# Performance work log

Measured on AMD Instinct MI355X. Metric: run time of the kernel, lower is better.

The kernel has to match this reference:

```python
import jax, jax.numpy as jnp
import numpy as np

B, S, D, H = 4, 1024, 1024, 16
HD = D // H
MAX_DIST, WIN, MAX_SPAN = 512, 256, 512
TEMP_SCALE = 0.01
EPS = 1e-5


def _ln(x, g, b):
    m = x.mean(-1, keepdims=True)
    v = ((x - m) ** 2).mean(-1, keepdims=True)
    return (x - m) * jax.lax.rsqrt(v + EPS) * g + b


def _heads(t):
    b, s, _ = t.shape
    return t.reshape(b, s, H, HD).transpose(0, 2, 1, 3)


def _merge(t):
    b, _, s, _ = t.shape
    return t.transpose(0, 2, 1, 3).reshape(b, s, D)


def _global_attn(x, Wq, bq, Wk, Wv, bv, Wo, bo):
    # MultiheadC with mask tensor passed -> is_causal=True SDPA (default 1/sqrt(HD) scale)
    q = _heads(x @ Wq.T + bq)
    k = _heads(x @ Wk.T)
    v = _heads(x @ Wv.T + bv)
    s = jnp.einsum('bhqd,bhkd->bhqk', q, k) / float(np.sqrt(HD))
    n = x.shape[1]
    causal = jnp.tril(jnp.ones((n, n), bool))
    s = jnp.where(causal, s, jnp.finfo(s.dtype).min)
    w = jax.nn.softmax(s, axis=-1)
    return _merge(jnp.einsum('bhqk,bhkd->bhqd', w, v)) @ Wo.T + bo


def _span_attn(q, k, v, temp):
    # AdaptiveSpan core: softmax(QK^T / temperature * head_dim**-0.25) V
    scale = HD ** -0.25
    qh, kh, vh = _heads(q), _heads(k), _heads(v)
    w = jax.nn.softmax(jnp.einsum('bhqd,bhkd->bhqk', qh, kh) / temp * scale, axis=-1)
    return _merge(jnp.einsum('bhqk,bhkd->bhqd', w, vh))


def _slide_win(local, span_mean, win, span_len, local_max):
    bx, sx, dx = local.shape
    temp = 1.0 + TEMP_SCALE * (1.0 - span_mean)  # sharpen=True branch
    outs = []
    for st in range(0, sx, win):  # static unrolled loop over windows (ragged slices)
        en = min(st + win, sx)
        wlen = en - st
        ks = max(0, st - span_len + win)
        ke = min(st + span_len, sx)
        klen = ke - ks
        eff = min(int(wlen * span_mean), wlen, klen, local_max)
        if eff <= 0:
            outs.append(jnp.zeros((bx, wlen, dx), local.dtype))
            continue
        o = _span_attn(local[:, st:st + eff], local[:, ks:ks + eff], local[:, ks:ks + eff], temp)
        if eff < wlen:
            o = jnp.concatenate([o, jnp.zeros((bx, wlen - eff, dx), local.dtype)], axis=1)
        outs.append(o)
    return jnp.concatenate(outs, axis=1)


def setup_inputs() -> dict:
    key = jax.random.key(0)
    ks = jax.random.split(key, 8)
    qkv_std = 1.0 / float(np.sqrt(HD))
    return {
        'x': jax.random.normal(ks[0], (B, S, D), jnp.float32),
        'ln_a_g': jnp.ones((D,), jnp.float32),
        'ln_a_b': jnp.zeros((D,), jnp.float32),
        'ln_b_g': jnp.ones((D,), jnp.float32),
        'ln_b_b': jnp.zeros((D,), jnp.float32),
        'Wq': jax.random.normal(ks[1], (D, D), jnp.float32) * qkv_std,
        'bq': jnp.zeros((D,), jnp.float32),
        'Wk': jax.random.normal(ks[2], (D, D), jnp.float32) * qkv_std,
        'Wv': jax.random.normal(ks[3], (D, D), jnp.float32) * qkv_std,
        'bv': jnp.zeros((D,), jnp.float32),
        'Wo': jax.random.normal(ks[4], (D, D), jnp.float32) * 0.02,
        'bo': jnp.zeros((D,), jnp.float32),
        'Wp': jax.random.normal(ks[5], (1, D), jnp.float32) * float(np.sqrt(2.0 / (D + 1))),
        'bp': jnp.zeros((1,), jnp.float32),
        'Wproj': jax.random.normal(ks[6], (D, 2 * D), jnp.float32) * 0.02,
        'bproj': jnp.zeros((D,), jnp.float32),
    }


def reference(x, ln_a_g, ln_a_b, ln_b_g, ln_b_b, Wq, bq, Wk, Wv, bv, Wo, bo, Wp, bp, Wproj, bproj):
    local = _ln(x, ln_a_g, ln_a_b)
    globe = _ln(x, ln_b_g, ln_b_b)
    globe_out = _global_attn(globe, Wq, bq, Wk, Wv, bv, Wo, bo)
    # Predictor: sigmoid(Linear(mean over seq))
    base_scale = jax.nn.sigmoid(globe_out.mean(axis=1) @ Wp.T + bp)  # [B, 1]
    span_scale = jnp.clip(base_scale, 0.0, 1.0)  # RL refine factor fixed at 1.0 (deterministic)
    span_mean = float(jnp.mean(span_scale))  # mirrors torch .item() host sync
    win = max(1, int(WIN * span_mean))
    span_len = max(1, int(MAX_SPAN * span_mean))
    local_max = min(MAX_DIST, span_len, win)
    local_out = _slide_win(local, span_mean, win, span_len, local_max)
    combined = jnp.concatenate([local_out, globe_out], axis=-1)
    return combined @ Wproj.T + bproj
```

## Files before the change

kernel.cpp:

```cpp
#include <hip/hip_runtime.h>
#include <math.h>

#define B_ 4
#define S_ 1024
#define D_ 1024
#define H_ 16
#define HD_ 64
#define BSD_ (B_*S_*D_)

using short8 = __attribute__((ext_vector_type(8))) short;
using f32x4  = __attribute__((ext_vector_type(4))) float;

#define MFMA16(a,b,c) __builtin_amdgcn_mfma_f32_16x16x32_bf16((a),(b),(c),0,0,0)

__device__ __forceinline__ ushort f2bf(float f) {
  uint u = __float_as_uint(f);
  return (ushort)((u + 0x7fffu + ((u >> 16) & 1u)) >> 16);
}
__device__ __forceinline__ float bf2f(ushort h) {
  return __uint_as_float(((uint)h) << 16);
}
__device__ __forceinline__ void split8(const float* p, short8* hi, short8* lo) {
  #pragma unroll
  for (int j = 0; j < 8; j++) {
    ushort h = f2bf(p[j]);
    (*hi)[j] = (short)h;
    (*lo)[j] = (short)f2bf(p[j] - bf2f(h));
  }
}
__device__ __forceinline__ void async_load16(const ushort* g, ushort* l) {
  __builtin_amdgcn_global_load_lds(
      (const __attribute__((address_space(1))) unsigned int*)g,
      (__attribute__((address_space(3))) unsigned int*)l, 16, 0, 0);
}

__device__ __forceinline__ float block_reduce_sum_256(float v, float* sbuf) {
  #pragma unroll
  for (int off = 32; off > 0; off >>= 1) v += __shfl_xor(v, off, 64);
  int lane = threadIdx.x & 63, wid = threadIdx.x >> 6;
  __syncthreads();
  if (lane == 0) sbuf[wid] = v;
  __syncthreads();
  return sbuf[0] + sbuf[1] + sbuf[2] + sbuf[3];
}

__global__ __launch_bounds__(256) void ln_kernel(const float* __restrict__ x,
                                                 const float* __restrict__ g,
                                                 const float* __restrict__ bta,
                                                 float* __restrict__ out) {
  __shared__ float sbuf[4];
  const int row = blockIdx.x;
  const float* xr = x + (size_t)row * D_;
  const int t = threadIdx.x;
  float v[4]; float s = 0.f;
  #pragma unroll
  for (int i = 0; i < 4; i++) { v[i] = xr[t + 256*i]; s += v[i]; }
  const float mean = block_reduce_sum_256(s, sbuf) * (1.0f/D_);
  float sq = 0.f;
  #pragma unroll
  for (int i = 0; i < 4; i++) { float d = v[i]-mean; sq += d*d; }
  const float var = block_reduce_sum_256(sq, sbuf) * (1.0f/D_);
  const float r = rsqrtf(var + 1e-5f);
  float* orow = out + (size_t)row * D_;
  #pragma unroll
  for (int i = 0; i < 4; i++) {
    int c = t + 256*i;
    orow[c] = (v[i]-mean)*r*g[c] + bta[c];
  }
}

__global__ __launch_bounds__(256) void ln_split_kernel(const float* __restrict__ x,
                                                       const float* __restrict__ g,
                                                       const float* __restrict__ bta,
                                                       ushort* __restrict__ out) {
  __shared__ float sbuf[4];
  const int row = blockIdx.x;
  const int t = threadIdx.x;
  const int c = t*4;
  const float* xr = x + (size_t)row * D_;
  float4 v = *(const float4*)(xr + c);
  float s = v.x + v.y + v.z + v.w;
  const float mean = block_reduce_sum_256(s, sbuf) * (1.0f/D_);
  float4 dv = make_float4(v.x-mean, v.y-mean, v.z-mean, v.w-mean);
  float sq = dv.x*dv.x + dv.y*dv.y + dv.z*dv.z + dv.w*dv.w;
  const float var = block_reduce_sum_256(sq, sbuf) * (1.0f/D_);
  const float r = rsqrtf(var + 1e-5f);
  float4 gg = *(const float4*)(g + c);
  float4 bb = *(const float4*)(bta + c);
  float n[4];
  n[0] = dv.x*r*gg.x + bb.x; n[1] = dv.y*r*gg.y + bb.y;
  n[2] = dv.z*r*gg.z + bb.z; n[3] = dv.w*r*gg.w + bb.w;
  ushort4 hi, lo;
  hi.x = f2bf(n[0]); hi.y = f2bf(n[1]); hi.z = f2bf(n[2]); hi.w = f2bf(n[3]);
  lo.x = f2bf(n[0]-bf2f(hi.x)); lo.y = f2bf(n[1]-bf2f(hi.y));
  lo.z = f2bf(n[2]-bf2f(hi.z)); lo.w = f2bf(n[3]-bf2f(hi.w));
  ushort* orow = out + (size_t)row*2048;
  *(ushort4*)(orow + c)        = hi;
  *(ushort4*)(orow + 1024 + c) = lo;
}

__global__ __launch_bounds__(256) void split_act_kernel(const float* __restrict__ in,
                                                        ushort* __restrict__ out) {
  const int idx = blockIdx.x*256 + threadIdx.x;
  const int row = idx >> 8;
  const int col4 = (idx & 255) << 2;
  const float4 a = *(const float4*)(in + (size_t)row*1024 + col4);
  ushort4 hi, lo;
  hi.x = f2bf(a.x); hi.y = f2bf(a.y); hi.z = f2bf(a.z); hi.w = f2bf(a.w);
  lo.x = f2bf(a.x - bf2f(hi.x)); lo.y = f2bf(a.y - bf2f(hi.y));
  lo.z = f2bf(a.z - bf2f(hi.z)); lo.w = f2bf(a.w - bf2f(hi.w));
  ushort* orow = out + (size_t)row*2048;
  *(ushort4*)(orow + col4)        = hi;
  *(ushort4*)(orow + 1024 + col4) = lo;
}

__global__ __launch_bounds__(256) void split_w3_kernel(const float* __restrict__ Wq,
                                                       const float* __restrict__ Wk,
                                                       const float* __restrict__ Wv,
                                                       const float* __restrict__ bq,
                                                       const float* __restrict__ bv,
                                                       ushort* __restrict__ out,
                                                       float* __restrict__ biascat) {
  const int idx = blockIdx.x*256 + threadIdx.x;
  const int n = idx >> 8;
  const int col4 = (idx & 255) << 2;
  const float* src = (n < 1024) ? (Wq + (size_t)n*1024)
                   : (n < 2048) ? (Wk + (size_t)(n-1024)*1024)
                                : (Wv + (size_t)(n-2048)*1024);
  const float4 a = *(const float4*)(src + col4);
  ushort4 hi, lo;
  hi.x = f2bf(a.x); hi.y = f2bf(a.y); hi.z = f2bf(a.z); hi.w = f2bf(a.w);
  lo.x = f2bf(a.x - bf2f(hi.x)); lo.y = f2bf(a.y - bf2f(hi.y));
  lo.z = f2bf(a.z - bf2f(hi.z)); lo.w = f2bf(a.w - bf2f(hi.w));
  ushort* orow = out + (size_t)n*2048;
  *(ushort4*)(orow + col4)        = hi;
  *(ushort4*)(orow + 1024 + col4) = lo;
  if (idx < 3072)
    biascat[idx] = (idx < 1024) ? bq[idx] : (idx < 2048) ? 0.f : bv[idx-2048];
}

__global__ __launch_bounds__(256) void split_w1_kernel(const float* __restrict__ W,
                                                       ushort* __restrict__ out) {
  const int idx = blockIdx.x*256 + threadIdx.x;
  const int n = idx >> 8;
  const int col4 = (idx & 255) << 2;
  const float4 a = *(const float4*)(W + (size_t)n*1024 + col4);
  ushort4 hi, lo;
  hi.x = f2bf(a.x); hi.y = f2bf(a.y); hi.z = f2bf(a.z); hi.w = f2bf(a.w);
  lo.x = f2bf(a.x - bf2f(hi.x)); lo.y = f2bf(a.y - bf2f(hi.y));
  lo.z = f2bf(a.z - bf2f(hi.z)); lo.w = f2bf(a.w - bf2f(hi.w));
  ushort* orow = out + (size_t)n*2048;
  *(ushort4*)(orow + col4)        = hi;
  *(ushort4*)(orow + 1024 + col4) = lo;
}

__global__ __launch_bounds__(256) void cvt_bf16_kernel(const float* __restrict__ in,
                                                       ushort* __restrict__ out,
                                                       int gprshift, int ostride, int ooff) {
  const int idx = blockIdx.x*256 + threadIdx.x;
  const int row = idx >> gprshift;
  const int col4 = (idx & ((1 << gprshift) - 1)) << 2;
  const int ncols = 4 << gprshift;
  const float4 a = *(const float4*)(in + (size_t)row*ncols + col4);
  ushort4 hi;
  hi.x = f2bf(a.x); hi.y = f2bf(a.y); hi.z = f2bf(a.z); hi.w = f2bf(a.w);
  *(ushort4*)(out + (size_t)row*ostride + ooff + col4) = hi;
}

__global__ __launch_bounds__(256) void mfma_gemm_qkv(
    const ushort* __restrict__ A, const ushort* __restrict__ Bw,
    const float* __restrict__ bias,
    ushort* __restrict__ Qsp, ushort* __restrict__ Ksp,
    ushort* __restrict__ Vth, ushort* __restrict__ Vtl, int Kh) {
  __shared__ __align__(16) ushort smem[17408];
  ushort* Ash = smem;
  ushort* Asl = smem + 4096;
  ushort* Bsh = smem + 8192;
  ushort* Bsl = smem + 12288;
  const int lda = 2*Kh;
  const int tid = threadIdx.x;
  const int bm = blockIdx.y * 128, bn = blockIdx.x * 128;
  const int wave = tid >> 6, lane = tid & 63;
  const int wm = wave >> 1, wn = wave & 1;
  const int lm = lane & 15, q = lane >> 4;
  const int lrow = lane >> 2;
  const int sw = (((lane & 3) ^ ((lane >> 3) & 3)) << 3);

  f32x4 acc[4][4];
  #pragma unroll
  for (int i = 0; i < 4; i++)
    #pragma unroll
    for (int j = 0; j < 4; j++)
      acc[i][j] = (f32x4){0.f,0.f,0.f,0.f};

  const ushort* Agh = A  + (size_t)(bm + wave*32 + lrow)*lda + sw;
  const ushort* Agl = Agh + Kh;
  const ushort* Bgh = Bw + (size_t)(bn + wave*32 + lrow)*lda + sw;
  const ushort* Bgl = Bgh + Kh;
  const size_t r16a = (size_t)16*lda;
  ushort* AhD0 = &Ash[(wave*32)*32];      ushort* AhD1 = &Ash[(wave*32+16)*32];
  ushort* AlD0 = &Asl[(wave*32)*32];      ushort* AlD1 = &Asl[(wave*32+16)*32];
  ushort* BhD0 = &Bsh[(wave*32)*32];      ushort* BhD1 = &Bsh[(wave*32+16)*32];
  ushort* BlD0 = &Bsl[(wave*32)*32];      ushort* BlD1 = &Bsl[(wave*32+16)*32];
  const int rsw  = ((q ^ ((lm >> 1) & 3)) << 3);
  const int aoff = (wm*64 + lm)*32 + rsw;
  const int boff = (wn*64 + lm)*32 + rsw;

  for (int k0 = 0; k0 < Kh; k0 += 32) {
    __syncthreads();
    async_load16(Agh + k0, AhD0);
    async_load16(Agh + r16a + k0, AhD1);
    async_load16(Agl + k0, AlD0);
    async_load16(Agl + r16a + k0, AlD1);
    async_load16(Bgh + k0, BhD0);
    async_load16(Bgh + r16a + k0, BhD1);
    async_load16(Bgl + k0, BlD0);
    async_load16(Bgl + r16a + k0, BlD1);
    __syncthreads();
    short8 ah[4], al[4], bh[4], bl[4];
    #pragma unroll
    for (int mt = 0; mt < 4; mt++) {
      ah[mt] = *(const short8*)&Ash[aoff + mt*512];
      al[mt] = *(const short8*)&Asl[aoff + mt*512];
    }
    #pragma unroll
    for (int nt = 0; nt < 4; nt++) {
      bh[nt] = *(const short8*)&Bsh[boff + nt*512];
      bl[nt] = *(const short8*)&Bsl[boff + nt*512];
    }
    #pragma unroll
    for (int mt = 0; mt < 4; mt++)
      #pragma unroll
      for (int nt = 0; nt < 4; nt++) {
        f32x4 a = acc[mt][nt];
        a = MFMA16(ah[mt], bh[nt], a);
        a = MFMA16(al[mt], bh[nt], a);
        a = MFMA16(ah[mt], bl[nt], a);
        acc[mt][nt] = a;
      }
  }

  const int b = bm >> 10, s0 = bm & 1023;
  if (blockIdx.x < 16) {
    ushort* dst = (blockIdx.x < 8) ? Qsp : Ksp;
    const int h = ((bn + wn*64) >> 6) & 15;
    #pragma unroll
    for (int mt = 0; mt < 4; mt++) {
      #pragma unroll
      for (int nt = 0; nt < 4; nt++) {
        const int n = bn + wn*64 + nt*16 + lm;
        const int d = nt*16 + lm;
        const float bb = bias[n];
        #pragma unroll
        for (int reg = 0; reg < 4; reg++) {
          const int s = s0 + wm*64 + mt*16 + q*4 + reg;
          const float val = acc[mt][nt][reg] + bb;
          const ushort hi = f2bf(val);
          const ushort lo = f2bf(val - bf2f(hi));
          ushort* rp = dst + ((size_t)((b*16 + h)*1024 + s))*128;
          rp[d] = hi; rp[64 + d] = lo;
        }
      }
    }
  } else {
    ushort* Th = smem;
    ushort* Tl = smem + 8704;
    #pragma unroll
    for (int c = 0; c < 2; c++) {
      __syncthreads();
      if (wn == c) {
        #pragma unroll
        for (int mt = 0; mt < 4; mt++)
          #pragma unroll
          for (int nt = 0; nt < 4; nt++) {
            const int nl = nt*16 + lm;
            const float bb = bias[bn + c*64 + nl];
            #pragma unroll
            for (int reg = 0; reg < 4; reg++) {
              const int sl = wm*64 + mt*16 + q*4 + reg;
              const float val = acc[mt][nt][reg] + bb;
              const ushort hi = f2bf(val);
              const ushort lo = f2bf(val - bf2f(hi));
              Th[nl*136 + sl] = hi;
              Tl[nl*136 + sl] = lo;
            }
          }
      }
      __syncthreads();
      const int nl = tid >> 2, s32 = (tid & 3)*32;
      const int h = ((bn - 2048 + c*64) >> 6) & 15;
      const size_t drow = ((size_t)((b*16 + h)*64 + nl))*1024 + s0 + s32;
      #pragma unroll
      for (int j = 0; j < 4; j++) {
        *(short8*)(Vth + drow + j*8) = *(const short8*)&Th[nl*136 + s32 + j*8];
        *(short8*)(Vtl + drow + j*8) = *(const short8*)&Tl[nl*136 + s32 + j*8];
      }
    }
  }
}

__global__ __launch_bounds__(256) void mfma_gemm2(
    const ushort* __restrict__ A, const ushort* __restrict__ Bw,
    const float* __restrict__ bias, float* __restrict__ C,
    int Kh, int ldc, ushort* __restrict__ aux) {
  __shared__ __align__(16) ushort Ash[128*32];
  __shared__ __align__(16) ushort Asl[128*32];
  __shared__ __align__(16) ushort Bsh[128*32];
  __shared__ __align__(16) ushort Bsl[128*32];
  const int lda = 2*Kh;
  const int tid = threadIdx.x;
  const int bm = blockIdx.y * 128, bn = blockIdx.x * 128;
  const int wave = tid >> 6, lane = tid & 63;
  const int wm = wave >> 1, wn = wave & 1;
  const int lm = lane & 15, q = lane >> 4;
  const int lrow = lane >> 2;
  const int sw = (((lane & 3) ^ ((lane >> 3) & 3)) << 3);

  f32x4 acc[4][4];
  #pragma unroll
  for (int i = 0; i < 4; i++)
    #pragma unroll
    for (int j = 0; j < 4; j++)
      acc[i][j] = (f32x4){0.f,0.f,0.f,0.f};

  const ushort* Agh = A  + (size_t)(bm + wave*32 + lrow)*lda + sw;
  const ushort* Agl = Agh + Kh;
  const ushort* Bgh = Bw + (size_t)(bn + wave*32 + lrow)*lda + sw;
  const ushort* Bgl = Bgh + Kh;
  const size_t r16a = (size_t)16*lda;
  ushort* AhD0 = &Ash[(wave*32)*32];      ushort* AhD1 = &Ash[(wave*32+16)*32];
  ushort* AlD0 = &Asl[(wave*32)*32];      ushort* AlD1 = &Asl[(wave*32+16)*32];
  ushort* BhD0 = &Bsh[(wave*32)*32];      ushort* BhD1 = &Bsh[(wave*32+16)*32];
  ushort* BlD0 = &Bsl[(wave*32)*32];      ushort* BlD1 = &Bsl[(wave*32+16)*32];
  const int rsw  = ((q ^ ((lm >> 1) & 3)) << 3);
  const int aoff = (wm*64 + lm)*32 + rsw;
  const int boff = (wn*64 + lm)*32 + rsw;

  for (int k0 = 0; k0 < Kh; k0 += 32) {
    __syncthreads();
    async_load16(Agh + k0, AhD0);
    async_load16(Agh + r16a + k0, AhD1);
    async_load16(Agl + k0, AlD0);
    async_load16(Agl + r16a + k0, AlD1);
    async_load16(Bgh + k0, BhD0);
    async_load16(Bgh + r16a + k0, BhD1);
    async_load16(Bgl + k0, BlD0);
    async_load16(Bgl + r16a + k0, BlD1);
    __syncthreads();
    short8 ah[4], al[4], bh[4], bl[4];
    #pragma unroll
    for (int mt = 0; mt < 4; mt++) {
      ah[mt] = *(const short8*)&Ash[aoff + mt*512];
      al[mt] = *(const short8*)&Asl[aoff + mt*512];
    }
    #pragma unroll
    for (int nt = 0; nt < 4; nt++) {
      bh[nt] = *(const short8*)&Bsh[boff + nt*512];
      bl[nt] = *(const short8*)&Bsl[boff + nt*512];
    }
    #pragma unroll
    for (int mt = 0; mt < 4; mt++)
      #pragma unroll
      for (int nt = 0; nt < 4; nt++) {
        f32x4 a = acc[mt][nt];
        a = MFMA16(ah[mt], bh[nt], a);
        a = MFMA16(al[mt], bh[nt], a);
        a = MFMA16(ah[mt], bl[nt], a);
        acc[mt][nt] = a;
      }
  }

  #pragma unroll
  for (int mt = 0; mt < 4; mt++) {
    #pragma unroll
    for (int nt = 0; nt < 4; nt++) {
      const int n = bn + wn*64 + nt*16 + lm;
      const float bb = bias ? bias[n] : 0.f;
      #pragma unroll
      for (int reg = 0; reg < 4; reg++) {
        const int m = bm + wm*64 + mt*16 + q*4 + reg;
        const float val = acc[mt][nt][reg] + bb;
        C[(size_t)m*ldc + n] = val;
        if (aux) aux[(size_t)m*2048 + 1024 + n] = f2bf(val);
      }
    }
  }
}

__global__ __launch_bounds__(256) void mfma_gemm(
    const ushort* __restrict__ A, const ushort* __restrict__ Bw,
    const float* __restrict__ bias, float* __restrict__ C,
    int K, int ldc) {
  __shared__ __align__(16) ushort As[128*32];
  __shared__ __align__(16) ushort Bs[128*32];
  const int tid = threadIdx.x;
  const int bm = blockIdx.y * 128, bn = blockIdx.x * 128;
  const int wave = tid >> 6, lane = tid & 63;
  const int wm = wave >> 1, wn = wave & 1;
  const int lm = lane & 15, q = lane >> 4;
  const int lrow = lane >> 2;
  const int sw = (((lane & 3) ^ ((lane >> 3) & 3)) << 3);

  f32x4 acc[4][4];
  #pragma unroll
  for (int i = 0; i < 4; i++)
    #pragma unroll
    for (int j = 0; j < 4; j++)
      acc[i][j] = (f32x4){0.f,0.f,0.f,0.f};

  const ushort* Ar0 = A  + (size_t)(bm + wave*32 + lrow)*K + sw;
  const ushort* Br0 = Bw + (size_t)(bn + wave*32 + lrow)*K + sw;
  const size_t r16 = (size_t)16*K;
  ushort* AsD0 = &As[(wave*32)*32];
  ushort* AsD1 = &As[(wave*32 + 16)*32];
  ushort* BsD0 = &Bs[(wave*32)*32];
  ushort* BsD1 = &Bs[(wave*32 + 16)*32];
  const int rsw  = ((q ^ ((lm >> 1) & 3)) << 3);
  const int aoff0 = (wm*64 + lm)*32 + rsw;
  const int boff0 = (wn*64 + lm)*32 + rsw;

  for (int k0 = 0; k0 < K; k0 += 32) {
    __syncthreads();
    async_load16(Ar0 + k0, AsD0);
    async_load16(Ar0 + r16 + k0, AsD1);
    async_load16(Br0 + k0, BsD0);
    async_load16(Br0 + r16 + k0, BsD1);
    __syncthreads();
    short8 af[4], bf[4];
    #pragma unroll
    for (int mt = 0; mt < 4; mt++) af[mt] = *(const short8*)&As[aoff0 + mt*512];
    #pragma unroll
    for (int nt = 0; nt < 4; nt++) bf[nt] = *(const short8*)&Bs[boff0 + nt*512];
    #pragma unroll
    for (int mt = 0; mt < 4; mt++)
      #pragma unroll
      for (int nt = 0; nt < 4; nt++)
        acc[mt][nt] = MFMA16(af[mt], bf[nt], acc[mt][nt]);
  }

  #pragma unroll
  for (int mt = 0; mt < 4; mt++) {
    #pragma unroll
    for (int nt = 0; nt < 4; nt++) {
      const int n = bn + wn*64 + nt*16 + lm;
      const float bb = bias ? bias[n] : 0.f;
      #pragma unroll
      for (int reg = 0; reg < 4; reg++) {
        const int m = bm + wm*64 + mt*16 + q*4 + reg;
        C[(size_t)m*ldc + n] = acc[mt][nt][reg] + bb;
      }
    }
  }
}

__global__ __launch_bounds__(256) void gattn_mfma(
    const ushort* __restrict__ Qsp, const ushort* __restrict__ Ksp,
    const ushort* __restrict__ Vth, const ushort* __restrict__ Vtl,
    float* __restrict__ O) {
  __shared__ __align__(16) ushort Kc[64*136];
  __shared__ __align__(16) ushort Vc[64*136];
  __shared__ __align__(16) float  Pf[64*66];
  const int bh = blockIdx.y;
  const int b = bh >> 4, h = bh & 15;
  const int tid = threadIdx.x;
  const int w = tid >> 6, lane = tid & 63;
  const int lm = lane & 15, q = lane >> 4;
  const ushort* Qb_ = Qsp + (size_t)bh * (1024*128);
  const ushort* Kb_ = Ksp + (size_t)bh * (1024*128);
  const ushort* Vhb = Vth + (size_t)bh * (64*1024);
  const ushort* Vlb = Vtl + (size_t)bh * (64*1024);

  for (int half = 0; half < 2; ++half) {
    const int qt = half ? blockIdx.x : 15 - blockIdx.x;
    short8 qh[2], ql[2];
    {
      const ushort* qr = Qb_ + (size_t)(qt*64 + w*16 + lm)*128 + q*8;
      qh[0] = *(const short8*)(qr);
      qh[1] = *(const short8*)(qr + 32);
      ql[0] = *(const short8*)(qr + 64);
      ql[1] = *(const short8*)(qr + 96);
    }
    f32x4 of[4];
    float mst[4], lst[4];
    #pragma unroll
    for (int nt = 0; nt < 4; nt++) of[nt] = (f32x4){0.f,0.f,0.f,0.f};
    #pragma unroll
    for (int rm = 0; rm < 4; rm++) { mst[rm] = -INFINITY; lst[rm] = 0.f; }
    const int nkt = qt + 1;
    for (int kt = 0; kt < nkt; ++kt) {
      __syncthreads();
      #pragma unroll
      for (int i = 0; i < 4; i++) {
        const int slot = i*256 + tid;
        const int row = slot >> 4, c8 = slot & 15;
        *(float4*)&Kc[row*136 + c8*8] =
            *(const float4*)(Kb_ + (size_t)(kt*64 + row)*128 + c8*8);
        const ushort* vsrc = ((c8 < 8) ? Vhb : Vlb) + (size_t)row*1024 + kt*64 + (c8&7)*8;
        *(float4*)&Vc[row*136 + c8*8] = *(const float4*)vsrc;
      }
      __syncthreads();
      f32x4 sS[4];
      #pragma unroll
      for (int nt = 0; nt < 4; nt++) {
        const ushort* kr = &Kc[(nt*16 + lm)*136 + q*8];
        const short8 kh0 = *(const short8*)(kr);
        const short8 kh1 = *(const short8*)(kr + 32);
        const short8 kl0 = *(const short8*)(kr + 64);
        const short8 kl1 = *(const short8*)(kr + 96);
        f32x4 a = (f32x4){0.f,0.f,0.f,0.f};
        a = MFMA16(qh[0], kh0, a);
        a = MFMA16(ql[0], kh0, a);
        a = MFMA16(qh[0], kl0, a);
        a = MFMA16(qh[1], kh1, a);
        a = MFMA16(ql[1], kh1, a);
        a = MFMA16(qh[1], kl1, a);
        sS[nt] = a;
      }
      const int ktbase = kt*64;
      const int qrow0 = qt*64 + w*16 + q*4;
      #pragma unroll
      for (int rm = 0; rm < 4; rm++) {
        const int qrow = qrow0 + rm;
        float v[4];
        #pragma unroll
        for (int nt = 0; nt < 4; nt++) {
          const int kcol = ktbase + nt*16 + lm;
          const float x = sS[nt][rm]*0.125f;
          v[nt] = (kcol <= qrow) ? x : -INFINITY;
        }
        float tm = fmaxf(fmaxf(v[0],v[1]), fmaxf(v[2],v[3]));
        #pragma unroll
        for (int off = 1; off < 16; off <<= 1) tm = fmaxf(tm, __shfl_xor(tm, off, 64));
        const float nm = fmaxf(mst[rm], tm);
        const float alpha = __expf(mst[rm] - nm);
        float ps = 0.f;
        #pragma unroll
        for (int nt = 0; nt < 4; nt++) {
          float p = __expf(v[nt] - nm);
          sS[nt][rm] = p;
          ps += p;
        }
        #pragma unroll
        for (int off = 1; off < 16; off <<= 1) ps += __shfl_xor(ps, off, 64);
        lst[rm] = lst[rm]*alpha + ps;
        mst[rm] = nm;
        #pragma unroll
        for (int nt = 0; nt < 4; nt++) of[nt][rm] *= alpha;
      }
      #pragma unroll
      for (int rm = 0; rm < 4; rm++)
        #pragma unroll
        for (int nt = 0; nt < 4; nt++)
          Pf[(w*16 + q*4 + rm)*66 + nt*16 + lm] = sS[nt][rm];
      short8 ph[2], pl[2];
      {
        const float* prow = &Pf[(w*16 + lm)*66];
        float pv[16];
        *(float4*)&pv[0]  = *(const float4*)(prow + q*8);
        *(float4*)&pv[4]  = *(const float4*)(prow + q*8 + 4);
        *(float4*)&pv[8]  = *(const float4*)(prow + 32 + q*8);
        *(float4*)&pv[12] = *(const float4*)(prow + 32 + q*8 + 4);
        split8(&pv[0], &ph[0], &pl[0]);
        split8(&pv[8], &ph[1], &pl[1]);
      }
      #pragma unroll
      for (int nt = 0; nt < 4; nt++) {
        const ushort* vr = &Vc[(nt*16 + lm)*136 + q*8];
        const short8 vh0 = *(const short8*)(vr);
        const short8 vh1 = *(const short8*)(vr + 32);
        const short8 vl0 = *(const short8*)(vr + 64);
        const short8 vl1 = *(const short8*)(vr + 96);
        f32x4 a = of[nt];
        a = MFMA16(ph[0], vh0, a);
        a = MFMA16(pl[0], vh0, a);
        a = MFMA16(ph[0], vl0, a);
        a = MFMA16(ph[1], vh1, a);
        a = MFMA16(pl[1], vh1, a);
        a = MFMA16(ph[1], vl1, a);
        of[nt] = a;
      }
    }
    #pragma unroll
    for (int rm = 0; rm < 4; rm++) {
      const float inv = 1.0f / lst[rm];
      const int s = qt*64 + w*16 + q*4 + rm;
      float* orow = O + ((size_t)(b*1024 + s))*1024 + h*64;
      #pragma unroll
      for (int nt = 0; nt < 4; nt++)
        orow[nt*16 + lm] = of[nt][rm] * inv;
    }
  }
}

__global__ __launch_bounds__(256) void seqmean1_kernel(const float* __restrict__ g,
                                                       float* __restrict__ part) {
  const int d = blockIdx.x*256 + threadIdx.x;
  const int sc = blockIdx.y;
  const int b = blockIdx.z;
  const float* p = g + ((size_t)b*S_ + sc*128)*D_ + d;
  float s = 0.f;
  #pragma unroll 4
  for (int i = 0; i < 128; i++) s += p[(size_t)i*D_];
  part[((size_t)(b*8 + sc))*D_ + d] = s;
}
__global__ __launch_bounds__(256) void seqmean2_kernel(const float* __restrict__ part,
                                                       float* __restrict__ mbd) {
  const int d = blockIdx.x*256 + threadIdx.x;
  const int b = blockIdx.y;
  float s = 0.f;
  #pragma unroll
  for (int i = 0; i < 8; i++) s += part[((size_t)(b*8 + i))*D_ + d];
  mbd[b*D_ + d] = s * (1.0f/S_);
}

__global__ __launch_bounds__(256) void predictor_kernel(
    const float* __restrict__ mbd, const float* __restrict__ Wp,
    const float* __restrict__ bp, float* __restrict__ fpar, int* __restrict__ ipar) {
  __shared__ float sbuf[4];
  __shared__ float sdots[4];
  const int tid = threadIdx.x;
  for (int b = 0; b < 4; b++) {
    float psum = 0.f;
    for (int d = tid; d < D_; d += 256) psum += mbd[b*D_ + d]*Wp[d];
    float tot = block_reduce_sum_256(psum, sbuf);
    if (tid == 0) sdots[b] = tot;
  }
  __syncthreads();
  if (tid == 0) {
    float smv = 0.f;
    for (int b = 0; b < 4; b++) {
      float z = sdots[b] + bp[0];
      smv += 1.0f/(1.0f + expf(-z));
    }
    smv *= 0.25f;
    int win = max(1, (int)(256.0f*smv));
    int span_len = max(1, (int)(512.0f*smv));
    int local_max = min(512, min(span_len, win));
    float temp = 1.0f + 0.01f*(1.0f - smv);
    int n_win = (S_ + win - 1)/win;
    fpar[0] = smv; fpar[1] = temp;
    ipar[0] = win; ipar[1] = span_len; ipar[2] = local_max; ipar[3] = n_win;
  }
}

#define LDP 68
__global__ __launch_bounds__(256) void lattn_kernel(
    const float* __restrict__ Lc, ushort* __restrict__ Out,
    const int* __restrict__ ip, const float* __restrict__ fpp) {
  __shared__ __align__(16) float Qs[HD_][LDP];
  __shared__ __align__(16) float KPs[64][LDP];
  __shared__ __align__(16) float Vs[64][LDP];
  const int n_win = ip[3];
  const int win = ip[0], span_len = ip[1], local_max = ip[2];
  const float sm = fpp[0], temp = fpp[1];
  const int bh = blockIdx.y;
  const int b = bh >> 4, h = bh & 15;
  const int tid = threadIdx.x;
  const int tx = tid & 15, ty = tid >> 4;
  const float sc = 0.35355339059327373f / temp;
  for (int w = blockIdx.x; w < n_win; w += gridDim.x) {
    const int st = w * win;
    const int en = min(st + win, S_); const int wlen = en - st;
    const int ks = max(0, st - span_len + win);
    const int ke = min(st + span_len, S_); const int klen = ke - ks;
    int eff = (int)((double)wlen * (double)sm);
    eff = min(min(eff, wlen), min(klen, local_max));
    if (eff > 0) {
      const int nt = (eff + 63) >> 6;
      for (int qt = 0; qt < nt; ++qt) {
        const int qn = min(64, eff - qt*64);
        __syncthreads();
        #pragma unroll
        for (int c = 0; c < 4; c++) {
          int f = tid + c*256;
          int r = f >> 4;
          int dc = (f & 15) << 2;
          float4 q4 = make_float4(0.f,0.f,0.f,0.f);
          if (r < qn) q4 = *(const float4*)(Lc + ((size_t)(b*S_ + st + qt*64 + r)) * D_ + h*HD_ + dc);
          Qs[dc+0][r]=q4.x; Qs[dc+1][r]=q4.y; Qs[dc+2][r]=q4.z; Qs[dc+3][r]=q4.w;
        }
        float o[4][4] = {{0.f,0.f,0.f,0.f},{0.f,0.f,0.f,0.f},{0.f,0.f,0.f,0.f},{0.f,0.f,0.f,0.f}};
        float mrow[4], lrow[4];
        #pragma unroll
        for (int i=0;i<4;i++){ mrow[i] = -INFINITY; lrow[i] = 0.f; }
        for (int kt = 0; kt < nt; ++kt) {
          const int kn = min(64, eff - kt*64);
          __syncthreads();
          #pragma unroll
          for (int c = 0; c < 4; c++) {
            int f = tid + c*256;
            int r = f >> 4;
            int dc = (f & 15) << 2;
            float4 k4 = make_float4(0.f,0.f,0.f,0.f);
            if (r < kn) k4 = *(const float4*)(Lc + ((size_t)(b*S_ + ks + kt*64 + r)) * D_ + h*HD_ + dc);
            KPs[dc+0][r]=k4.x; KPs[dc+1][r]=k4.y; KPs[dc+2][r]=k4.z; KPs[dc+3][r]=k4.w;
            *(float4*)&Vs[r][dc] = k4;
          }
          __syncthreads();
          float s[4][4] = {{0.f,0.f,0.f,0.f},{0.f,0.f,0.f,0.f},{0.f,0.f,0.f,0.f},{0.f,0.f,0.f,0.f}};
          #pragma unroll 8
          for (int d = 0; d < HD_; ++d) {
            const float4 a  = *(const float4*)&Qs[d][ty*4];
            const float4 bb = *(const float4*)&KPs[d][tx*4];
            const float av[4]={a.x,a.y,a.z,a.w};
            const float bv[4]={bb.x,bb.y,bb.z,bb.w};
            #pragma unroll
            for (int i=0;i<4;i++)
              #pragma unroll
              for (int j=0;j<4;j++)
                s[i][j] += av[i]*bv[j];
          }
          #pragma unroll
          for (int i=0;i<4;i++) {
            #pragma unroll
            for (int j=0;j<4;j++) {
              float lg = s[i][j]*sc;
              if (kt*64 + tx*4 + j >= eff) lg = -INFINITY;
              s[i][j] = lg;
            }
          }
          #pragma unroll
          for (int i=0;i<4;i++) {
            float tm = fmaxf(fmaxf(s[i][0],s[i][1]), fmaxf(s[i][2],s[i][3]));
            #pragma unroll
            for (int off=1; off<16; off<<=1) tm = fmaxf(tm, __shfl_xor(tm, off, 64));
            const float nm = fmaxf(mrow[i], tm);
            const float alpha = __expf(mrow[i]-nm);
            float ps = 0.f;
            #pragma unroll
            for (int j=0;j<4;j++){ float p = __expf(s[i][j]-nm); s[i][j]=p; ps += p; }
            #pragma unroll
            for (int off=1; off<16; off<<=1) ps += __shfl_xor(ps, off, 64);
            lrow[i] = lrow[i]*alpha + ps;
            mrow[i] = nm;
            #pragma unroll
            for (int j=0;j<4;j++) o[i][j] *= alpha;
          }
          __syncthreads();
          #pragma unroll
          for (int i=0;i<4;i++)
            #pragma unroll
            for (int j=0;j<4;j++)
              KPs[tx*4+j][ty*4+i] = s[i][j];
          __syncthreads();
          #pragma unroll 8
          for (int kk = 0; kk < 64; ++kk) {
            const float4 a  = *(const float4*)&KPs[kk][ty*4];
            const float4 bb = *(const float4*)&Vs[kk][tx*4];
            const float av[4]={a.x,a.y,a.z,a.w};
            const float bv[4]={bb.x,bb.y,bb.z,bb.w};
            #pragma unroll
            for (int i=0;i<4;i++)
              #pragma unroll
              for (int j=0;j<4;j++)
                o[i][j] += av[i]*bv[j];
          }
        }
        #pragma unroll
        for (int i=0;i<4;i++){
          const int r = ty*4 + i;
          if (r < qn) {
            const float inv = 1.0f / lrow[i];
            ushort4 ov;
            ov.x = f2bf(o[i][0]*inv); ov.y = f2bf(o[i][1]*inv);
            ov.z = f2bf(o[i][2]*inv); ov.w = f2bf(o[i][3]*inv);
            *(ushort4*)(Out + ((size_t)(b*S_ + st + qt*64 + r)) * 2048 + h*HD_ + tx*4) = ov;
          }
        }
      }
    }
    const ushort4 z = {0,0,0,0};
    for (int r = max(eff, 0) + ty; r < wlen; r += 16)
      *(ushort4*)(Out + ((size_t)(b*S_ + st + r)) * 2048 + h*HD_ + tx*4) = z;
  }
}

extern "C" void kernel_launch(void* const* d_in, const int* in_sizes, int n_in,
                              void* d_out, int out_size, void* d_ws, size_t ws_size,
                              hipStream_t stream) {
  const float* x      = (const float*)d_in[0];
  const float* ln_a_g = (const float*)d_in[1];
  const float* ln_a_b = (const float*)d_in[2];
  const float* ln_b_g = (const float*)d_in[3];
  const float* ln_b_b = (const float*)d_in[4];
  const float* Wq     = (const float*)d_in[5];
  const float* bq     = (const float*)d_in[6];
  const float* Wk     = (const float*)d_in[7];
  const float* Wv     = (const float*)d_in[8];
  const float* bv     = (const float*)d_in[9];
  const float* Wo     = (const float*)d_in[10];
  const float* bo     = (const float*)d_in[11];
  const float* Wp     = (const float*)d_in[12];
  const float* bp     = (const float*)d_in[13];
  const float* Wproj  = (const float*)d_in[14];
  const float* bproj  = (const float*)d_in[15];
  float* out = (float*)d_out;
  float* ws  = (float*)d_ws;
  ushort* wsu = (ushort*)d_ws;

  ushort* Qsp = wsu;
  ushort* Ksp = wsu + 8388608;
  ushort* Vth = wsu + 16777216;
  ushort* Vtl = wsu + 20971520;
  float* buf0 = ws + 12582912;
  float* glo  = ws + 16777216;
  float* loc  = ws + 20971520;
  float* biascat = ws + 25165824;
  float* mbd  = biascat + 4096;
  float* fpar = mbd + 4096;
  int*   ipar = (int*)(fpar + 8);
  ushort* Acat  = (ushort*)(ws + 25182208);
  ushort* Bqkv  = Acat + 12582912;
  ushort* Bo    = Bqkv + 9437184;
  float*  part = (float*)Acat;
  ushort* A3  = wsu;
  ushort* B3  = wsu + 8388608;

  const dim3 blk(256);

  ln_split_kernel<<<dim3(B_*S_), blk, 0, stream>>>(x, ln_b_g, ln_b_b, Acat);
  split_w3_kernel<<<dim3(3072), blk, 0, stream>>>(Wq, Wk, Wv, bq, bv, Bqkv, biascat);
  mfma_gemm_qkv<<<dim3(24, 32), blk, 0, stream>>>(Acat, Bqkv, biascat,
                                                  Qsp, Ksp, Vth, Vtl, 1024);
  gattn_mfma<<<dim3(8, 64), blk, 0, stream>>>(Qsp, Ksp, Vth, Vtl, buf0);
  split_act_kernel<<<dim3(4096), blk, 0, stream>>>(buf0, Acat);
  split_w1_kernel<<<dim3(1024), blk, 0, stream>>>(Wo, Bo);
  mfma_gemm2<<<dim3(8, 32), blk, 0, stream>>>(Acat, Bo, bo, glo, 1024, 1024, A3);
  seqmean1_kernel<<<dim3(4, 8, B_), blk, 0, stream>>>(glo, part);
  seqmean2_kernel<<<dim3(4, B_), blk, 0, stream>>>(part, mbd);
  predictor_kernel<<<dim3(1), blk, 0, stream>>>(mbd, Wp, bp, fpar, ipar);
  ln_kernel<<<dim3(B_*S_), blk, 0, stream>>>(x, ln_a_g, ln_a_b, loc);
  lattn_kernel<<<dim3(64, B_*H_), blk, 0, stream>>>(loc, A3, ipar, fpar);
  cvt_bf16_kernel<<<dim3(2048), blk, 0, stream>>>(Wproj, B3, 9, 2048, 0);
  mfma_gemm<<<dim3(8, 32), blk, 0, stream>>>(A3, B3, bproj, out, 2048, 1024);
}
```

Baseline: 481.4 us.

## Fuse bf16 split into attention epilogue and share K/V tiles across paired query tiles

The global attention kernel now writes its normalized output directly as hi/lo bf16 pairs into the GEMM input buffer, removing the separate split kernel and the fp32 intermediate round trip. It also processes both of a block's query tiles in one key loop, so each K/V tile is staged into shared memory once and serves both tiles. This doubles the live accumulator and Q fragment state per thread, which may raise register pressure and lower occupancy.

Result: no change. 480.0 us (-0.3%).

```diff
diff --git a/kernel.cpp b/kernel.cpp
--- a/kernel.cpp
+++ b/kernel.cpp
@@ -97,21 +97,6 @@
   ushort* orow = out + (size_t)row*2048;
   *(ushort4*)(orow + c)        = hi;
   *(ushort4*)(orow + 1024 + c) = lo;
-}
-
-__global__ __launch_bounds__(256) void split_act_kernel(const float* __restrict__ in,
-                                                        ushort* __restrict__ out) {
-  const int idx = blockIdx.x*256 + threadIdx.x;
-  const int row = idx >> 8;
-  const int col4 = (idx & 255) << 2;
-  const float4 a = *(const float4*)(in + (size_t)row*1024 + col4);
-  ushort4 hi, lo;
-  hi.x = f2bf(a.x); hi.y = f2bf(a.y); hi.z = f2bf(a.z); hi.w = f2bf(a.w);
-  lo.x = f2bf(a.x - bf2f(hi.x)); lo.y = f2bf(a.y - bf2f(hi.y));
-  lo.z = f2bf(a.z - bf2f(hi.z)); lo.w = f2bf(a.w - bf2f(hi.w));
-  ushort* orow = out + (size_t)row*2048;
-  *(ushort4*)(orow + col4)        = hi;
-  *(ushort4*)(orow + 1024 + col4) = lo;
 }
 
 __global__ __launch_bounds__(256) void split_w3_kernel(const float* __restrict__ Wq,
@@ -453,10 +438,97 @@
   }
 }
 
+__device__ __forceinline__ void attn_unit(
+    int qt, int kt, int w, int lm, int q,
+    const short8 qh[2], const short8 ql[2],
+    const ushort* Kc, const ushort* Vc, float* Pf,
+    f32x4 of[4], float mst[4], float lst[4]) {
+  f32x4 sS[4];
+  #pragma unroll
+  for (int nt = 0; nt < 4; nt++) {
+    const ushort* kr = &Kc[(nt*16 + lm)*136 + q*8];
+    const short8 kh0 = *(const short8*)(kr);
+    const short8 kh1 = *(const short8*)(kr + 32);
+    const short8 kl0 = *(const short8*)(kr + 64);
+    const short8 kl1 = *(const short8*)(kr + 96);
+    f32x4 a = (f32x4){0.f,0.f,0.f,0.f};
+    a = MFMA16(qh[0], kh0, a);
+    a = MFMA16(ql[0], kh0, a);
+    a = MFMA16(qh[0], kl0, a);
+    a = MFMA16(qh[1], kh1, a);
+    a = MFMA16(ql[1], kh1, a);
+    a = MFMA16(qh[1], kl1, a);
+    sS[nt] = a;
+  }
+  const int ktbase = kt*64;
+  const int qrow0 = qt*64 + w*16 + q*4;
+  #pragma unroll
+  for (int rm = 0; rm < 4; rm++) {
+    const int qrow = qrow0 + rm;
+    float v[4];
+    #pragma unroll
+    for (int nt = 0; nt < 4; nt++) {
+      const int kcol = ktbase + nt*16 + lm;
+      const float x = sS[nt][rm]*0.125f;
+      v[nt] = (kcol <= qrow) ? x : -INFINITY;
+    }
+    float tm = fmaxf(fmaxf(v[0],v[1]), fmaxf(v[2],v[3]));
+    #pragma unroll
+    for (int off = 1; off < 16; off <<= 1) tm = fmaxf(tm, __shfl_xor(tm, off, 64));
+    const float nm = fmaxf(mst[rm], tm);
+    const float alpha = __expf(mst[rm] - nm);
+    float ps = 0.f;
+    #pragma unroll
+    for (int nt = 0; nt < 4; nt++) {
+      float p = __expf(v[nt] - nm);
+      sS[nt][rm] = p;
+      ps += p;
+    }
+    #pragma unroll
+    for (int off = 1; off < 16; off <<= 1) ps += __shfl_xor(ps, off, 64);
+    lst[rm] = lst[rm]*alpha + ps;
+    mst[rm] = nm;
+    #pragma unroll
+    for (int nt = 0; nt < 4; nt++) of[nt][rm] *= alpha;
+  }
+  #pragma unroll
+  for (int rm = 0; rm < 4; rm++)
+    #pragma unroll
+    for (int nt = 0; nt < 4; nt++)
+      Pf[(w*16 + q*4 + rm)*66 + nt*16 + lm] = sS[nt][rm];
+  short8 ph[2], pl[2];
+  {
+    const float* prow = &Pf[(w*16 + lm)*66];
+    float pv[16];
+    *(float4*)&pv[0]  = *(const float4*)(prow + q*8);
+    *(float4*)&pv[4]  = *(const float4*)(prow + q*8 + 4);
+    *(float4*)&pv[8]  = *(const float4*)(prow + 32 + q*8);
+    *(float4*)&pv[12] = *(const float4*)(prow + 32 + q*8 + 4);
+    split8(&pv[0], &ph[0], &pl[0]);
+    split8(&pv[8], &ph[1], &pl[1]);
+  }
+  #pragma unroll
+  for (int nt = 0; nt < 4; nt++) {
+    const ushort* vr = &Vc[(nt*16 + lm)*136 + q*8];
+    const short8 vh0 = *(const short8*)(vr);
+    const short8 vh1 = *(const short8*)(vr + 32);
+    const short8 vl0 = *(const short8*)(vr + 64);
+    const short8 vl1 = *(const short8*)(vr + 96);
+    f32x4 a = of[nt];
+    a = MFMA16(ph[0], vh0, a);
+    a = MFMA16(pl[0], vh0, a);
+    a = MFMA16(ph[0], vl0, a);
+    a = MFMA16(ph[1], vh1, a);
+    a = MFMA16(pl[1], vh1, a);
+    a = MFMA16(ph[1], vl1, a);
+    of[nt] = a;
+  }
+}
+
 __global__ __launch_bounds__(256) void gattn_mfma(
     const ushort* __restrict__ Qsp, const ushort* __restrict__ Ksp,
     const ushort* __restrict__ Vth, const ushort* __restrict__ Vtl,
-    float* __restrict__ O) {
+    ushort* __restrict__ Aout) {
   __shared__ __align__(16) ushort Kc[64*136];
   __shared__ __align__(16) ushort Vc[64*136];
   __shared__ __align__(16) float  Pf[64*66];
@@ -469,125 +541,73 @@
   const ushort* Kb_ = Ksp + (size_t)bh * (1024*128);
   const ushort* Vhb = Vth + (size_t)bh * (64*1024);
   const ushort* Vlb = Vtl + (size_t)bh * (64*1024);
-
-  for (int half = 0; half < 2; ++half) {
-    const int qt = half ? blockIdx.x : 15 - blockIdx.x;
-    short8 qh[2], ql[2];
-    {
-      const ushort* qr = Qb_ + (size_t)(qt*64 + w*16 + lm)*128 + q*8;
-      qh[0] = *(const short8*)(qr);
-      qh[1] = *(const short8*)(qr + 32);
-      ql[0] = *(const short8*)(qr + 64);
-      ql[1] = *(const short8*)(qr + 96);
-    }
-    f32x4 of[4];
-    float mst[4], lst[4];
-    #pragma unroll
-    for (int nt = 0; nt < 4; nt++) of[nt] = (f32x4){0.f,0.f,0.f,0.f};
-    #pragma unroll
-    for (int rm = 0; rm < 4; rm++) { mst[rm] = -INFINITY; lst[rm] = 0.f; }
-    const int nkt = qt + 1;
-    for (int kt = 0; kt < nkt; ++kt) {
-      __syncthreads();
-      #pragma unroll
-      for (int i = 0; i < 4; i++) {
-        const int slot = i*256 + tid;
-        const int row = slot >> 4, c8 = slot & 15;
-        *(float4*)&Kc[row*136 + c8*8] =
-            *(const float4*)(Kb_ + (size_t)(kt*64 + row)*128 + c8*8);
-        const ushort* vsrc = ((c8 < 8) ? Vhb : Vlb) + (size_t)row*1024 + kt*64 + (c8&7)*8;
-        *(float4*)&Vc[row*136 + c8*8] = *(const float4*)vsrc;
-      }
-      __syncthreads();
-      f32x4 sS[4];
-      #pragma unroll
-      for (int nt = 0; nt < 4; nt++) {
-        const ushort* kr = &Kc[(nt*16 + lm)*136 + q*8];
-        const short8 kh0 = *(const short8*)(kr);
-        const short8 kh1 = *(const short8*)(kr + 32);
-        const short8 kl0 = *(const short8*)(kr + 64);
-        const short8 kl1 = *(const short8*)(kr + 96);
-        f32x4 a = (f32x4){0.f,0.f,0.f,0.f};
-        a = MFMA16(qh[0], kh0, a);
-        a = MFMA16(ql[0], kh0, a);
-        a = MFMA16(qh[0], kl0, a);
-        a = MFMA16(qh[1], kh1, a);
-        a = MFMA16(ql[1], kh1, a);
-        a = MFMA16(qh[1], kl1, a);
-        sS[nt] = a;
-      }
-      const int ktbase = kt*64;
-      const int qrow0 = qt*64 + w*16 + q*4;
-      #pragma unroll
-      for (int rm = 0; rm < 4; rm++) {
-        const int qrow = qrow0 + rm;
-        float v[4];
-        #pragma unroll
-        for (int nt = 0; nt < 4; nt++) {
-          const int kcol = ktbase + nt*16 + lm;
-          const float x = sS[nt][rm]*0.125f;
-          v[nt] = (kcol <= qrow) ? x : -INFINITY;
-        }
-        float tm = fmaxf(fmaxf(v[0],v[1]), fmaxf(v[2],v[3]));
-        #pragma unroll
-        for (int off = 1; off < 16; off <<= 1) tm = fmaxf(tm, __shfl_xor(tm, off, 64));
-        const float nm = fmaxf(mst[rm], tm);
-        const float alpha = __expf(mst[rm] - nm);
-        float ps = 0.f;
-        #pragma unroll
-        for (int nt = 0; nt < 4; nt++) {
-          float p = __expf(v[nt] - nm);
-          sS[nt][rm] = p;
-          ps += p;
-        }
-        #pragma unroll
-        for (int off = 1; off < 16; off <<= 1) ps += __shfl_xor(ps, off, 64);
-        lst[rm] = lst[rm]*alpha + ps;
-        mst[rm] = nm;
-        #pragma unroll
-        for (int nt = 0; nt < 4; nt++) of[nt][rm] *= alpha;
-      }
-      #pragma unroll
-      for (int rm = 0; rm < 4; rm++)
-        #pragma unroll
-        for (int nt = 0; nt < 4; nt++)
-          Pf[(w*16 + q*4 + rm)*66 + nt*16 + lm] = sS[nt][rm];
-      short8 ph[2], pl[2];
-      {
-        const float* prow = &Pf[(w*16 + lm)*66];
-        float pv[16];
-        *(float4*)&pv[0]  = *(const float4*)(prow + q*8);
-        *(float4*)&pv[4]  = *(const float4*)(prow + q*8 + 4);
-        *(float4*)&pv[8]  = *(const float4*)(prow + 32 + q*8);
-        *(float4*)&pv[12] = *(const float4*)(prow + 32 + q*8 + 4);
-        split8(&pv[0], &ph[0], &pl[0]);
-        split8(&pv[8], &ph[1], &pl[1]);
-      }
-      #pragma unroll
-      for (int nt = 0; nt < 4; nt++) {
-        const ushort* vr = &Vc[(nt*16 + lm)*136 + q*8];
-        const short8 vh0 = *(const short8*)(vr);
-        const short8 vh1 = *(const short8*)(vr + 32);
-        const short8 vl0 = *(const short8*)(vr + 64);
-        const short8 vl1 = *(const short8*)(vr + 96);
-        f32x4 a = of[nt];
-        a = MFMA16(ph[0], vh0, a);
-        a = MFMA16(pl[0], vh0, a);
-        a = MFMA16(ph[0], vl0, a);
-        a = MFMA16(ph[1], vh1, a);
-        a = MFMA16(pl[1], vh1, a);
-        a = MFMA16(ph[1], vl1, a);
-        of[nt] = a;
-      }
-    }
-    #pragma unroll
-    for (int rm = 0; rm < 4; rm++) {
-      const float inv = 1.0f / lst[rm];
-      const int s = qt*64 + w*16 + q*4 + rm;
-      float* orow = O + ((size_t)(b*1024 + s))*1024 + h*64;
-      #pragma unroll
-      for (int nt = 0; nt < 4; nt++)
-        orow[nt*16 + lm] = of[nt][rm] * inv;
+  const int qtA = 15 - blockIdx.x;
+  const int qtB = blockIdx.x;
+
+  short8 qhA[2], qlA[2], qhB[2], qlB[2];
+  {
+    const ushort* qr = Qb_ + (size_t)(qtA*64 + w*16 + lm)*128 + q*8;
+    qhA[0] = *(const short8*)(qr);
+    qhA[1] = *(const short8*)(qr + 32);
+    qlA[0] = *(const short8*)(qr + 64);
+    qlA[1] = *(const short8*)(qr + 96);
+    const ushort* qr2 = Qb_ + (size_t)(qtB*64 + w*16 + lm)*128 + q*8;
+    qhB[0] = *(const short8*)(qr2);
+    qhB[1] = *(const short8*)(qr2 + 32);
+    qlB[0] = *(const short8*)(qr2 + 64);
+    qlB[1] = *(const short8*)(qr2 + 96);
+  }
+  f32x4 ofA[4], ofB[4];
+  float mstA[4], lstA[4], mstB[4], lstB[4];
+  #pragma unroll
+  for (int nt = 0; nt < 4; nt++) {
+    ofA[nt] = (f32x4){0.f,0.f,0.f,0.f};
+    ofB[nt] = (f32x4){0.f,0.f,0.f,0.f};
+  }
+  #pragma unroll
+  for (int rm = 0; rm < 4; rm++) {
+    mstA[rm] = -INFINITY; lstA[rm] = 0.f;
+    mstB[rm] = -INFINITY; lstB[rm] = 0.f;
+  }
+
+  for (int kt = 0; kt <= qtA; ++kt) {
+    __syncthreads();
+    #pragma unroll
+    for (int i = 0; i < 4; i++) {
+      const int slot = i*256 + tid;
+      const int row = slot >> 4, c8 = slot & 15;
+      *(float4*)&Kc[row*136 + c8*8] =
+          *(const float4*)(Kb_ + (size_t)(kt*64 + row)*128 + c8*8);
+      const ushort* vsrc = ((c8 < 8) ? Vhb : Vlb) + (size_t)row*1024 + kt*64 + (c8&7)*8;
+      *(float4*)&Vc[row*136 + c8*8] = *(const float4*)vsrc;
+    }
+    __syncthreads();
+    attn_unit(qtA, kt, w, lm, q, qhA, qlA, Kc, Vc, Pf, ofA, mstA, lstA);
+    if (kt <= qtB)
+      attn_unit(qtB, kt, w, lm, q, qhB, qlB, Kc, Vc, Pf, ofB, mstB, lstB);
+  }
+
+  #pragma unroll
+  for (int rm = 0; rm < 4; rm++) {
+    const float invA = 1.0f / lstA[rm];
+    const int sA = qtA*64 + w*16 + q*4 + rm;
+    ushort* arow = Aout + ((size_t)(b*1024 + sA))*2048 + h*64;
+    #pragma unroll
+    for (int nt = 0; nt < 4; nt++) {
+      const float val = ofA[nt][rm] * invA;
+      const ushort hi = f2bf(val);
+      arow[nt*16 + lm] = hi;
+      arow[1024 + nt*16 + lm] = f2bf(val - bf2f(hi));
+    }
+    const float invB = 1.0f / lstB[rm];
+    const int sB = qtB*64 + w*16 + q*4 + rm;
+    ushort* brow = Aout + ((size_t)(b*1024 + sB))*2048 + h*64;
+    #pragma unroll
+    for (int nt = 0; nt < 4; nt++) {
+      const float val = ofB[nt][rm] * invB;
+      const ushort hi = f2bf(val);
+      brow[nt*16 + lm] = hi;
+      brow[1024 + nt*16 + lm] = f2bf(val - bf2f(hi));
     }
   }
 }
@@ -802,7 +822,6 @@
   ushort* Ksp = wsu + 8388608;
   ushort* Vth = wsu + 16777216;
   ushort* Vtl = wsu + 20971520;
-  float* buf0 = ws + 12582912;
   float* glo  = ws + 16777216;
   float* loc  = ws + 20971520;
   float* biascat = ws + 25165824;
@@ -822,8 +841,7 @@
   split_w3_kernel<<<dim3(3072), blk, 0, stream>>>(Wq, Wk, Wv, bq, bv, Bqkv, biascat);
   mfma_gemm_qkv<<<dim3(24, 32), blk, 0, stream>>>(Acat, Bqkv, biascat,
                                                   Qsp, Ksp, Vth, Vtl, 1024);
-  gattn_mfma<<<dim3(8, 64), blk, 0, stream>>>(Qsp, Ksp, Vth, Vtl, buf0);
-  split_act_kernel<<<dim3(4096), blk, 0, stream>>>(buf0, Acat);
+  gattn_mfma<<<dim3(8, 64), blk, 0, stream>>>(Qsp, Ksp, Vth, Vtl, Acat);
   split_w1_kernel<<<dim3(1024), blk, 0, stream>>>(Wo, Bo);
   mfma_gemm2<<<dim3(8, 32), blk, 0, stream>>>(Acat, Bo, bo, glo, 1024, 1024, A3);
   seqmean1_kernel<<<dim3(4, 8, B_), blk, 0, stream>>>(glo, part);
```
